# Kernel tuning notes

Hardware: AMD Instinct MI355X
Metric: run time of the kernel (lower is better)

The kernel has to match this reference:

```python
import jax, jax.numpy as jnp
import numpy as np
from jax import lax

EPS = 1e-5

# ---- 1-bit activation quantizer with straight-through estimator ----
@jax.custom_vjp
def ste_sign(x):
    return jnp.sign(x)

def _ste_sign_fwd(x):
    return jnp.sign(x), x

def _ste_sign_bwd(res, g):
    x = res
    # clipped STE: pass gradient where |x| <= 1
    return (g * (jnp.abs(x) <= 1.0).astype(g.dtype),)

ste_sign.defvjp(_ste_sign_fwd, _ste_sign_bwd)

# ---- 1-bit weight binarization: sign(w) * per-out-channel mean(|w|), STE ----
@jax.custom_vjp
def bin_weight(w):
    alpha = jnp.mean(jnp.abs(w), axis=(1, 2, 3), keepdims=True)  # [O,1,1,1]
    return jnp.sign(w) * alpha

def _bw_fwd(w):
    return bin_weight(w), w

def _bw_bwd(res, g):
    w = res
    # weight_clip=1: straight-through inside the clip range
    return (g * (jnp.abs(w) <= 1.0).astype(g.dtype),)

bin_weight.defvjp(_bw_fwd, _bw_bwd)

def conv3x3(x, w):
    # zero padding=1, stride=1, NCHW / OIHW
    return lax.conv_general_dilated(
        x, w, window_strides=(1, 1), padding=((1, 1), (1, 1)),
        dimension_numbers=('NCHW', 'OIHW', 'NCHW'))

def batchnorm(x, gamma, beta):
    # training-mode BN with batch statistics over (N,H,W)
    mean = jnp.mean(x, axis=(0, 2, 3), keepdims=True)
    var = jnp.var(x, axis=(0, 2, 3), keepdims=True)
    xn = (x - mean) * lax.rsqrt(var + EPS)
    return xn * gamma[None, :, None, None] + beta[None, :, None, None]


def setup_inputs() -> dict:
    key = jax.random.key(0)
    k1, k2, k3 = jax.random.split(key, 3)
    N, C, H, W = 32, 256, 56, 56
    return {
        'x': jax.random.normal(k1, (N, C, H, W), dtype=jnp.float32),
        'w1': jax.random.normal(k2, (C, C, 3, 3), dtype=jnp.float32) * 0.05,
        'gamma1': jnp.ones((C,), dtype=jnp.float32),
        'beta1': jnp.zeros((C,), dtype=jnp.float32),
        'w2': jax.random.normal(k3, (C, C, 3, 3), dtype=jnp.float32) * 0.05,
        'gamma2': jnp.ones((C,), dtype=jnp.float32),
        'beta2': jnp.zeros((C,), dtype=jnp.float32),
    }


def reference(x, w1, gamma1, beta1, w2, gamma2, beta2):
    identity = x
    out = ste_sign(x)                       # quantized activation (1-bit, signed)
    out = conv3x3(out, bin_weight(w1))      # BinConv 3x3, stride 1
    out = batchnorm(out, gamma1, beta1)
    out = ste_sign(out)
    out = conv3x3(out, bin_weight(w2))
    out = batchnorm(out, gamma2, beta2)
    return out + identity                   # residual add (downsample=None)
```

## Files before the change

### kernel.cpp

```cpp
#include <hip/hip_runtime.h>
#include <stdint.h>

#define NB 32
#define CH 256
#define HH 56
#define WW 56
#define HWSZ (HH*WW)
#define NPIX (NB*HWSZ)
#define HP 58
#define WP 58
#define PADPIX (NB*HP*WP)
#define NTAPS 9
#define KKE (CH*NTAPS)
#define NPIXD 100352.0
#define WQ_CONV (NTAPS*8*8*64*16)
#define HSTRIDE 272

typedef int int4v  __attribute__((ext_vector_type(4)));
typedef int int16v __attribute__((ext_vector_type(16)));

__global__ void init_kernel(long long* __restrict__ sums8) {
    int t = blockIdx.x*256 + threadIdx.x;
    if (t < 2*8*512) sums8[t] = 0;
}

__global__ void wqpack_kernel(const float* __restrict__ w1, const float* __restrict__ w2,
                              int8_t* __restrict__ wq) {
    int t = blockIdx.x*256 + threadIdx.x;
    int conv = blockIdx.y;
    const float* w = conv ? w2 : w1;
    int lane = t & 63;
    int g = t >> 6;
    int nb = g & 7, h = g >> 3;
    int ks = h & 7, tap = h >> 3;
    int o = nb*32 + (lane & 31);
    int cin0 = ks*32 + (lane >> 5)*16;
    int wd[4];
    #pragma unroll
    for (int q = 0; q < 4; ++q) {
        int wv = 0;
        #pragma unroll
        for (int j = 0; j < 4; ++j) {
            float v = w[(size_t)(o*CH + cin0 + q*4 + j)*NTAPS + tap];
            int s = (v > 0.f) ? 1 : ((v < 0.f) ? -1 : 0);
            wv |= (s & 0xff) << (8*j);
        }
        wd[q] = wv;
    }
    *(int4v*)(wq + (size_t)conv*WQ_CONV + (size_t)t*16) = (int4v){wd[0], wd[1], wd[2], wd[3]};
}

__global__ void alpha_kernel(const float* __restrict__ w1, const float* __restrict__ w2,
                             float* __restrict__ alpha) {
    int o = blockIdx.x; int conv = blockIdx.y;
    const float* w = conv ? w2 : w1;
    float s = 0.f;
    for (int i = threadIdx.x; i < KKE; i += 256) s += fabsf(w[(size_t)o*KKE + i]);
    for (int off = 32; off; off >>= 1) s += __shfl_down(s, off);
    __shared__ float l[4];
    int lane = threadIdx.x & 63, wv = threadIdx.x >> 6;
    if (lane == 0) l[wv] = s;
    __syncthreads();
    if (threadIdx.x == 0) alpha[conv*CH + o] = (l[0]+l[1]+l[2]+l[3]) * (1.f/KKE);
}

__global__ void pack_x_kernel(const float* __restrict__ x, int8_t* __restrict__ apad) {
    int p = blockIdx.x*256 + threadIdx.x;
    if (p >= PADPIX) return;
    int n  = p / (HP*WP);
    int r  = p - n*(HP*WP);
    int hp = r / WP, wp = r - hp*WP;
    int4v* dst = (int4v*)(apad + (size_t)p*CH);
    if (hp >= 1 && hp <= HH && wp >= 1 && wp <= WW) {
        const float* xb = x + (size_t)n*CH*HWSZ + (hp-1)*WW + (wp-1);
        #pragma unroll 2
        for (int c16 = 0; c16 < 16; ++c16) {
            int wd[4];
            #pragma unroll
            for (int q = 0; q < 4; ++q) {
                int wv = 0;
                #pragma unroll
                for (int j = 0; j < 4; ++j) {
                    float v = xb[(size_t)(c16*16 + q*4 + j)*HWSZ];
                    int s = (v > 0.f) ? 1 : ((v < 0.f) ? -1 : 0);
                    wv |= (s & 0xff) << (8*j);
                }
                wd[q] = wv;
            }
            dst[c16] = (int4v){wd[0], wd[1], wd[2], wd[3]};
        }
    } else {
        int4v z = {0,0,0,0};
        #pragma unroll
        for (int c16 = 0; c16 < 16; ++c16) dst[c16] = z;
    }
}

__global__ void pack_s_kernel(const int16_t* __restrict__ cnt,
                              const float* __restrict__ ab,
                              int8_t* __restrict__ apad) {
    int p = blockIdx.x*256 + threadIdx.x;
    if (p >= PADPIX) return;
    int n  = p / (HP*WP);
    int r  = p - n*(HP*WP);
    int hp = r / WP, wp = r - hp*WP;
    int4v* dst = (int4v*)(apad + (size_t)p*CH);
    if (hp >= 1 && hp <= HH && wp >= 1 && wp <= WW) {
        const int4v* cb = (const int4v*)(cnt + ((size_t)n*HWSZ + (hp-1)*WW + (wp-1))*CH);
        #pragma unroll 2
        for (int c16 = 0; c16 < 16; ++c16) {
            int4v u0 = cb[c16*2], u1 = cb[c16*2+1];
            int wd[4];
            #pragma unroll
            for (int q = 0; q < 4; ++q) {
                int wv = 0;
                #pragma unroll
                for (int j = 0; j < 4; ++j) {
                    int e = q*4 + j;
                    int word = (e < 8) ? u0[e >> 1] : u1[(e-8) >> 1];
                    int sval = (e & 1) ? (word >> 16) : ((word << 16) >> 16);
                    int ch = c16*16 + e;
                    float v = fmaf(ab[ch], (float)sval, ab[CH + ch]);
                    int s = (v > 0.f) ? 1 : ((v < 0.f) ? -1 : 0);
                    wv |= (s & 0xff) << (8*j);
                }
                wd[q] = wv;
            }
            dst[c16] = (int4v){wd[0], wd[1], wd[2], wd[3]};
        }
    } else {
        int4v z = {0,0,0,0};
        #pragma unroll
        for (int c16 = 0; c16 < 16; ++c16) dst[c16] = z;
    }
}

#define AOFF(IT) (((((IT)>>3)/3)*10 + (((IT)>>3)%3))*HSTRIDE + ((IT)&7)*32)

#define CONV_BODY \
    __syncthreads(); \
    int lane = t & 63; \
    int nbp = __builtin_amdgcn_readfirstlane(t >> 6); \
    int kh = lane >> 5, lr = lane & 31; \
    int r0 = lr >> 3, c0 = lr & 7; \
    int base0 = (r0*10 + c0)*HSTRIDE + kh*16; \
    int base1 = base0 + 40*HSTRIDE; \
    const int8_t* wp0 = wq + nbp*2048 + lane*16; \
    const int8_t* wp1 = wp0 + 1024; \
    int16v acc00, acc01, acc10, acc11; \
    _Pragma("unroll") \
    for (int i = 0; i < 16; ++i) { acc00[i]=0; acc01[i]=0; acc10[i]=0; acc11[i]=0; } \
    _Pragma("unroll") \
    for (int it = 0; it < 72; ++it) { \
        int4v a0 = *(const int4v*)&halo[base0 + AOFF(it)]; \
        int4v a1 = *(const int4v*)&halo[base1 + AOFF(it)]; \
        int4v b0 = *(const int4v*)(wp0 + it*8192); \
        int4v b1 = *(const int4v*)(wp1 + it*8192); \
        acc00 = __builtin_amdgcn_mfma_i32_32x32x32_i8(a0, b0, acc00, 0,0,0); \
        acc01 = __builtin_amdgcn_mfma_i32_32x32x32_i8(a0, b1, acc01, 0,0,0); \
        acc10 = __builtin_amdgcn_mfma_i32_32x32x32_i8(a1, b0, acc10, 0,0,0); \
        acc11 = __builtin_amdgcn_mfma_i32_32x32x32_i8(a1, b1, acc11, 0,0,0); \
    } \
    { \
        int s1a = 0, s2a = 0, s1b = 0, s2b = 0; \
        _Pragma("unroll") \
        for (int reg = 0; reg < 16; ++reg) { \
            int row_ = (reg & 3) + 8*(reg >> 2) + 4*kh; \
            _Pragma("unroll") \
            for (int m = 0; m < 2; ++m) { \
                int pm_ = m*32 + row_; \
                int rr_ = pm_ >> 3, cc_ = pm_ & 7; \
                size_t pbase_ = (size_t)((n0*HH + ty*8 + rr_)*WW + tx*8 + cc_)*CH; \
                int v0 = (m ? acc10[reg] : acc00[reg]); \
                int v1 = (m ? acc11[reg] : acc01[reg]); \
                cnt[pbase_ + (nbp*2+0)*32 + lr] = (int16_t)v0; \
                cnt[pbase_ + (nbp*2+1)*32 + lr] = (int16_t)v1; \
                s1a += v0; s2a += v0*v0; s1b += v1; s2b += v1*v1; \
            } \
        } \
        s1a += __shfl_down(s1a, 32); s2a += __shfl_down(s2a, 32); \
        s1b += __shfl_down(s1b, 32); s2b += __shfl_down(s2b, 32); \
        if (lane < 32) { \
            long long* sp = sums8 + (size_t)(b & 7)*512; \
            int ch0 = nbp*64 + lr, ch1 = ch0 + 32; \
            atomicAdd((unsigned long long*)&sp[2*ch0],   (unsigned long long)(long long)s1a); \
            atomicAdd((unsigned long long*)&sp[2*ch0+1], (unsigned long long)(long long)s2a); \
            atomicAdd((unsigned long long*)&sp[2*ch1],   (unsigned long long)(long long)s1b); \
            atomicAdd((unsigned long long*)&sp[2*ch1+1], (unsigned long long)(long long)s2b); \
        } \
    }

__global__ __launch_bounds__(256, 3) void conv_kernel(
        const int8_t* __restrict__ apad, const int8_t* __restrict__ wq,
        int16_t* __restrict__ cnt, long long* __restrict__ sums8) {
    __shared__ __attribute__((aligned(16))) int8_t halo[100*HSTRIDE];
    int b = blockIdx.x;
    int tile = b % 49, n0 = b / 49;
    int ty = tile / 7, tx = tile % 7;
    int t = threadIdx.x;

    #pragma unroll 1
    for (int j = 0; j < 7; ++j) {
        int idx = t + j*256;
        if (idx < 1600) {
            int pix = idx >> 4, c16 = idx & 15;
            int dr = pix / 10, dc = pix - dr*10;
            const int4v* src = (const int4v*)(apad +
                ((size_t)((n0*HP + ty*8+dr)*WP + tx*8+dc))*CH + c16*16);
            *(int4v*)&halo[pix*HSTRIDE + c16*16] = *src;
        }
    }
    CONV_BODY
}

__global__ __launch_bounds__(256, 3) void conv2_kernel(
        const int16_t* __restrict__ src16, const float* __restrict__ ab,
        const int8_t* __restrict__ wq,
        int16_t* __restrict__ cnt, long long* __restrict__ sums8) {
    __shared__ __attribute__((aligned(16))) int8_t halo[100*HSTRIDE];
    int b = blockIdx.x;
    int tile = b % 49, n0 = b / 49;
    int ty = tile / 7, tx = tile % 7;
    int t = threadIdx.x;

    {
        int c16s = t & 15;
        #pragma unroll 1
        for (int k = 0; k < 7; ++k) {
            int pix = (t >> 4) + k*16;
            if (pix < 100) {
                int dr = pix / 10, dc = pix - dr*10;
                int hi = ty*8 + dr - 1, wi = tx*8 + dc - 1;
                int4v outv = {0,0,0,0};
                if ((unsigned)hi < (unsigned)HH && (unsigned)wi < (unsigned)WW) {
                    const int16_t* sp = src16 + ((size_t)(n0*HH + hi)*WW + wi)*CH + c16s*16;
                    int4v u0 = *(const int4v*)sp;
                    int4v u1 = *(const int4v*)(sp + 8);
                    int wd[4];
                    #pragma unroll
                    for (int q = 0; q < 4; ++q) {
                        int wv = 0;
                        #pragma unroll
                        for (int j = 0; j < 4; ++j) {
                            int e = q*4 + j;
                            int word = (e < 8) ? u0[e >> 1] : u1[(e-8) >> 1];
                            int sval = (e & 1) ? (word >> 16) : ((word << 16) >> 16);
                            int ch = c16s*16 + e;
                            float v = fmaf(ab[ch], (float)sval, ab[CH + ch]);
                            int s = (v > 0.f) ? 1 : ((v < 0.f) ? -1 : 0);
                            wv |= (s & 0xff) << (8*j);
                        }
                        wd[q] = wv;
                    }
                    outv = (int4v){wd[0], wd[1], wd[2], wd[3]};
                }
                *(int4v*)&halo[pix*HSTRIDE + c16s*16] = outv;
            }
        }
    }
    CONV_BODY
}

__global__ void bncoef_kernel(const long long* __restrict__ sums8,
                              const float* __restrict__ alpha,
                              const float* __restrict__ gamma, const float* __restrict__ beta,
                              float* __restrict__ ab) {
    int o = threadIdx.x;
    long long S1i = 0, S2i = 0;
    #pragma unroll
    for (int k = 0; k < 8; ++k) {
        S1i += sums8[(size_t)k*512 + 2*o];
        S2i += sums8[(size_t)k*512 + 2*o + 1];
    }
    double S1 = (double)S1i, S2 = (double)S2i;
    double mean = S1 / NPIXD;
    double var  = S2 / NPIXD - mean*mean;
    double al   = (double)alpha[o];
    double rs   = 1.0 / sqrt(al*al*var + 1e-5);
    double a    = (double)gamma[o] * al * rs;
    ab[o]      = (float)a;
    ab[CH + o] = (float)((double)beta[o] - a*mean);
}

__global__ __launch_bounds__(256) void final_kernel(const int16_t* __restrict__ cnt,
        const float* __restrict__ x, const float* __restrict__ ab, float* __restrict__ out) {
    __shared__ int4v lsd4[64*32];
    int8_t* lb = (int8_t*)lsd4;
    int b = blockIdx.x;
    int n = b / 49, tile = b - n*49;
    int p0 = tile * 64;
    int t = threadIdx.x;
    const int4v* src = (const int4v*)(cnt + ((size_t)n*HWSZ + p0)*CH);
    #pragma unroll
    for (int j = 0; j < 8; ++j) {
        int c = t + j*256;
        int pix = c >> 5, c16 = c & 31;
        *(int4v*)&lb[pix*512 + ((c16*16) ^ ((pix & 15) << 4))] = src[c];
    }
    __syncthreads();
    int pixL = t & 63;
    int cb = (t >> 6) * 64;
    #pragma unroll 1
    for (int i = 0; i < 8; ++i) {
        int ch0 = cb + i*8;
        int4v v = *(const int4v*)&lb[pixL*512 + ((ch0*2) ^ ((pixL & 15) << 4))];
        #pragma unroll
        for (int j = 0; j < 8; ++j) {
            int ch = ch0 + j;
            int word = v[j >> 1];
            int sval = (j & 1) ? (word >> 16) : ((word << 16) >> 16);
            size_t g = (size_t)(n*CH + ch)*HWSZ + p0 + pixL;
            out[g] = fmaf(ab[ch], (float)sval, ab[CH + ch]) + x[g];
        }
    }
}

extern "C" void kernel_launch(void* const* d_in, const int* in_sizes, int n_in,
                              void* d_out, int out_size, void* d_ws, size_t ws_size,
                              hipStream_t stream) {
    const float* x  = (const float*)d_in[0];
    const float* w1 = (const float*)d_in[1];
    const float* g1 = (const float*)d_in[2];
    const float* b1 = (const float*)d_in[3];
    const float* w2 = (const float*)d_in[4];
    const float* g2 = (const float*)d_in[5];
    const float* b2 = (const float*)d_in[6];
    float* out = (float*)d_out;

    char* ws = (char*)d_ws;
    size_t off = 0;
    auto alloc = [&](size_t nbytes) { char* pp = ws + off; off = (off + nbytes + 255) & ~(size_t)255; return pp; };
    int8_t*   apad  = (int8_t*)alloc((size_t)PADPIX*CH);
    int16_t*  cnt1  = (int16_t*)alloc((size_t)NPIX*CH*2);
    int8_t*   wq    = (int8_t*)alloc((size_t)2*WQ_CONV);
    float*    alpha = (float*)alloc((size_t)2*CH*4);
    long long* sums8 = (long long*)alloc((size_t)2*8*512*8);
    float*    ab    = (float*)alloc((size_t)2*2*CH*4);

    size_t cntBytes = (size_t)NPIX*CH*2;
    bool fused = (ws_size >= off + cntBytes + 4096);
    int16_t* cnt2 = fused ? (int16_t*)alloc(cntBytes) : cnt1;

    init_kernel<<<32, 256, 0, stream>>>(sums8);
    wqpack_kernel<<<dim3(144, 2), 256, 0, stream>>>(w1, w2, wq);
    alpha_kernel<<<dim3(CH, 2), 256, 0, stream>>>(w1, w2, alpha);
    pack_x_kernel<<<(PADPIX + 255)/256, 256, 0, stream>>>(x, apad);

    conv_kernel<<<1568, 256, 0, stream>>>(apad, wq, cnt1, sums8);
    bncoef_kernel<<<1, CH, 0, stream>>>(sums8, alpha, g1, b1, ab);

    if (fused) {
        conv2_kernel<<<1568, 256, 0, stream>>>(cnt1, ab, wq + WQ_CONV, cnt2, sums8 + 8*512);
    } else {
        pack_s_kernel<<<(PADPIX + 255)/256, 256, 0, stream>>>(cnt1, ab, apad);
        conv_kernel<<<1568, 256, 0, stream>>>(apad, wq + WQ_CONV, cnt2, sums8 + 8*512);
    }
    bncoef_kernel<<<1, CH, 0, stream>>>(sums8 + 8*512, alpha + CH, g2, b2, ab + 2*CH);

    final_kernel<<<1568, 256, 0, stream>>>(cnt2, x, ab + 2*CH, out);
}
```

Measured before the change: 248.6 us.

## Software-pipeline weight loads per tap and XOR-swizzle halo LDS layout

The fully unrolled 72-step MFMA loop becomes a 9-tap loop. Each tap is split into two halves with double-buffered weight registers, so the next half's global weight loads are issued while the current half's MFMAs run. The halo shared-memory layout gains an XOR swizzle of the 16-byte channel chunks keyed on pixel row, meant to reduce LDS bank conflicts on the A-operand reads. Launch bounds drop from 3 to 2 blocks per CU to allow the larger register footprint, at the cost of occupancy.

```diff
diff --git a/kernel.cpp b/kernel.cpp
--- a/kernel.cpp
+++ b/kernel.cpp
@@ -135,7 +135,11 @@
     }
 }
 
-#define AOFF(IT) (((((IT)>>3)/3)*10 + (((IT)>>3)%3))*HSTRIDE + ((IT)&7)*32)
+#define MFMA8(AQ0, AQ1, B0, B1) \
+    acc00 = __builtin_amdgcn_mfma_i32_32x32x32_i8(AQ0, B0, acc00, 0,0,0); \
+    acc01 = __builtin_amdgcn_mfma_i32_32x32x32_i8(AQ0, B1, acc01, 0,0,0); \
+    acc10 = __builtin_amdgcn_mfma_i32_32x32x32_i8(AQ1, B0, acc10, 0,0,0); \
+    acc11 = __builtin_amdgcn_mfma_i32_32x32x32_i8(AQ1, B1, acc11, 0,0,0);
 
 #define CONV_BODY \
     __syncthreads(); \
@@ -143,23 +147,59 @@
     int nbp = __builtin_amdgcn_readfirstlane(t >> 6); \
     int kh = lane >> 5, lr = lane & 31; \
     int r0 = lr >> 3, c0 = lr & 7; \
-    int base0 = (r0*10 + c0)*HSTRIDE + kh*16; \
-    int base1 = base0 + 40*HSTRIDE; \
+    int pix0 = r0*10 + c0; \
     const int8_t* wp0 = wq + nbp*2048 + lane*16; \
-    const int8_t* wp1 = wp0 + 1024; \
     int16v acc00, acc01, acc10, acc11; \
     _Pragma("unroll") \
     for (int i = 0; i < 16; ++i) { acc00[i]=0; acc01[i]=0; acc10[i]=0; acc11[i]=0; } \
-    _Pragma("unroll") \
-    for (int it = 0; it < 72; ++it) { \
-        int4v a0 = *(const int4v*)&halo[base0 + AOFF(it)]; \
-        int4v a1 = *(const int4v*)&halo[base1 + AOFF(it)]; \
-        int4v b0 = *(const int4v*)(wp0 + it*8192); \
-        int4v b1 = *(const int4v*)(wp1 + it*8192); \
-        acc00 = __builtin_amdgcn_mfma_i32_32x32x32_i8(a0, b0, acc00, 0,0,0); \
-        acc01 = __builtin_amdgcn_mfma_i32_32x32x32_i8(a0, b1, acc01, 0,0,0); \
-        acc10 = __builtin_amdgcn_mfma_i32_32x32x32_i8(a1, b0, acc10, 0,0,0); \
-        acc11 = __builtin_amdgcn_mfma_i32_32x32x32_i8(a1, b1, acc11, 0,0,0); \
+    int4v bA0,bA1,bA2,bA3,bA4,bA5,bA6,bA7,bB0,bB1,bB2,bB3,bB4,bB5,bB6,bB7; \
+    bA0 = *(const int4v*)(wp0);             bA1 = *(const int4v*)(wp0 + 1024); \
+    bA2 = *(const int4v*)(wp0 + 8192);      bA3 = *(const int4v*)(wp0 + 9216); \
+    bA4 = *(const int4v*)(wp0 + 16384);     bA5 = *(const int4v*)(wp0 + 17408); \
+    bA6 = *(const int4v*)(wp0 + 24576);     bA7 = *(const int4v*)(wp0 + 25600); \
+    _Pragma("unroll 1") \
+    for (int tt = 0; tt < 9; ++tt) { \
+        int dh = (tt*11) >> 5;                \
+        int trow = dh*7 + tt;                 \
+        int pr0 = pix0 + trow, pr1 = pr0 + 40; \
+        int sw0 = (pr0 >> 3) & 7, sw1 = (pr1 >> 3) & 7; \
+        int rb0 = pr0*HSTRIDE, rb1 = pr1*HSTRIDE; \
+        int e00 = rb0 + (((0+kh) ^ sw0) << 4), e01 = rb0 + (((2+kh) ^ sw0) << 4); \
+        int e02 = rb0 + (((4+kh) ^ sw0) << 4), e03 = rb0 + (((6+kh) ^ sw0) << 4); \
+        int e10 = rb1 + (((0+kh) ^ sw1) << 4), e11 = rb1 + (((2+kh) ^ sw1) << 4); \
+        int e12 = rb1 + (((4+kh) ^ sw1) << 4), e13 = rb1 + (((6+kh) ^ sw1) << 4); \
+        const int8_t* wt = wp0 + tt*65536; \
+         \
+        bB0 = *(const int4v*)(wt + 32768);      bB1 = *(const int4v*)(wt + 33792); \
+        bB2 = *(const int4v*)(wt + 40960);      bB3 = *(const int4v*)(wt + 41984); \
+        bB4 = *(const int4v*)(wt + 49152);      bB5 = *(const int4v*)(wt + 50176); \
+        bB6 = *(const int4v*)(wt + 57344);      bB7 = *(const int4v*)(wt + 58368); \
+        { \
+            int4v a00 = *(const int4v*)&halo[e00], a10 = *(const int4v*)&halo[e10]; \
+            int4v a01 = *(const int4v*)&halo[e01], a11 = *(const int4v*)&halo[e11]; \
+            int4v a02 = *(const int4v*)&halo[e02], a12 = *(const int4v*)&halo[e12]; \
+            int4v a03 = *(const int4v*)&halo[e03], a13 = *(const int4v*)&halo[e13]; \
+            MFMA8(a00, a10, bA0, bA1) \
+            MFMA8(a01, a11, bA2, bA3) \
+            MFMA8(a02, a12, bA4, bA5) \
+            MFMA8(a03, a13, bA6, bA7) \
+        } \
+         \
+        const int8_t* wn = (tt < 8) ? (wt + 65536) : wp0; \
+        bA0 = *(const int4v*)(wn);              bA1 = *(const int4v*)(wn + 1024); \
+        bA2 = *(const int4v*)(wn + 8192);       bA3 = *(const int4v*)(wn + 9216); \
+        bA4 = *(const int4v*)(wn + 16384);      bA5 = *(const int4v*)(wn + 17408); \
+        bA6 = *(const int4v*)(wn + 24576);      bA7 = *(const int4v*)(wn + 25600); \
+        { \
+            int4v a00 = *(const int4v*)&halo[e00+128], a10 = *(const int4v*)&halo[e10+128]; \
+            int4v a01 = *(const int4v*)&halo[e01+128], a11 = *(const int4v*)&halo[e11+128]; \
+            int4v a02 = *(const int4v*)&halo[e02+128], a12 = *(const int4v*)&halo[e12+128]; \
+            int4v a03 = *(const int4v*)&halo[e03+128], a13 = *(const int4v*)&halo[e13+128]; \
+            MFMA8(a00, a10, bB0, bB1) \
+            MFMA8(a01, a11, bB2, bB3) \
+            MFMA8(a02, a12, bB4, bB5) \
+            MFMA8(a03, a13, bB6, bB7) \
+        } \
     } \
     { \
         int s1a = 0, s2a = 0, s1b = 0, s2b = 0; \
@@ -190,7 +230,7 @@
         } \
     }
 
-__global__ __launch_bounds__(256, 3) void conv_kernel(
+__global__ __launch_bounds__(256, 2) void conv_kernel(
         const int8_t* __restrict__ apad, const int8_t* __restrict__ wq,
         int16_t* __restrict__ cnt, long long* __restrict__ sums8) {
     __shared__ __attribute__((aligned(16))) int8_t halo[100*HSTRIDE];
@@ -207,13 +247,13 @@
             int dr = pix / 10, dc = pix - dr*10;
             const int4v* src = (const int4v*)(apad +
                 ((size_t)((n0*HP + ty*8+dr)*WP + tx*8+dc))*CH + c16*16);
-            *(int4v*)&halo[pix*HSTRIDE + c16*16] = *src;
+            *(int4v*)&halo[pix*HSTRIDE + ((c16 ^ ((pix >> 3) & 7)) << 4)] = *src;
         }
     }
     CONV_BODY
 }
 
-__global__ __launch_bounds__(256, 3) void conv2_kernel(
+__global__ __launch_bounds__(256, 2) void conv2_kernel(
         const int16_t* __restrict__ src16, const float* __restrict__ ab,
         const int8_t* __restrict__ wq,
         int16_t* __restrict__ cnt, long long* __restrict__ sums8) {
@@ -254,7 +294,7 @@
                     }
                     outv = (int4v){wd[0], wd[1], wd[2], wd[3]};
                 }
-                *(int4v*)&halo[pix*HSTRIDE + c16s*16] = outv;
+                *(int4v*)&halo[pix*HSTRIDE + ((c16s ^ ((pix >> 3) & 7)) << 4)] = outv;
             }
         }
     }
```

New measurement: 249.7 us. About the same (+0.5%).
